# Kernel optimization log

Hardware: AMD Instinct MI355X
Metric: run time of the kernel (lower is better)

The kernel has to match this reference:

```python
import jax, jax.numpy as jnp
import numpy as np

B, N, DEG = 16, 2048, 16          # graphs, nodes per graph, avg out-degree
C_IN, HID, K = 64, 128, 32        # in_channels, hidden_channels, out_channels (clusters)
NT = B * N                        # total nodes
E = NT * DEG                      # total edges
GN_EPS = 1e-5


def setup_inputs() -> dict:
    key = jax.random.key(0)
    ks = jax.random.split(key, 6)
    x = jax.random.normal(ks[0], (NT, C_IN), jnp.float32)
    # within-graph random edges (sorted batch => node i belongs to graph i // N)
    src_l = jax.random.randint(ks[1], (E,), 0, N)
    dst_l = jax.random.randint(ks[2], (E,), 0, N)
    gid = jnp.repeat(jnp.arange(B, dtype=jnp.int32), N * DEG)
    edge_index = jnp.stack([gid * N + src_l, gid * N + dst_l]).astype(jnp.int32)
    batch = jnp.repeat(jnp.arange(B, dtype=jnp.int32), N)
    return dict(
        x=x, edge_index=edge_index, batch=batch,
        gn_weight=jnp.ones((C_IN,), jnp.float32),
        gn_bias=jnp.zeros((C_IN,), jnp.float32),
        gn_mean_scale=jnp.ones((C_IN,), jnp.float32),
        w1=jax.random.normal(ks[3], (C_IN, HID), jnp.float32) / np.float32(np.sqrt(C_IN)),
        b1=jnp.zeros((HID,), jnp.float32),
        w2=jax.random.normal(ks[4], (HID, K), jnp.float32) / np.float32(np.sqrt(HID)),
        b2=jnp.zeros((K,), jnp.float32),
    )


def reference(x, gn_weight, gn_bias, gn_mean_scale, w1, b1, w2, b2, edge_index, batch):
    # ---- GraphNorm (per-graph mean/var with learnable mean scale) ----
    ones_n = jnp.ones((NT,), x.dtype)
    cnt = jax.ops.segment_sum(ones_n, batch, num_segments=B)[:, None]        # [B,1]
    mean = jax.ops.segment_sum(x, batch, num_segments=B) / cnt              # [B,C]
    xm = x - gn_mean_scale * mean[batch]
    var = jax.ops.segment_sum(xm * xm, batch, num_segments=B) / cnt         # [B,C]
    h = gn_weight * xm / jnp.sqrt(var + GN_EPS)[batch] + gn_bias            # [NT,C_IN]

    # ---- GCNConv (add self-loops, symmetric D^-1/2 (A+I) D^-1/2) ----
    src, dst = edge_index[0], edge_index[1]
    loop = jnp.arange(NT, dtype=src.dtype)
    src_l = jnp.concatenate([src, loop])
    dst_l = jnp.concatenate([dst, loop])
    deg = jax.ops.segment_sum(jnp.ones_like(src_l, x.dtype), dst_l, num_segments=NT)
    dinv = jnp.where(deg > 0, jax.lax.rsqrt(deg), 0.0)
    norm = dinv[src_l] * dinv[dst_l]                                        # [E+NT]
    hw = h @ w1                                                             # [NT,HID]
    h = jax.ops.segment_sum(norm[:, None] * hw[src_l], dst_l, num_segments=NT) + b1
    h = jax.nn.selu(h)

    # ---- to_dense_batch / to_dense_adj (uniform graph sizes -> mask all True) ----
    xd = h.reshape(B, N, HID)                                               # [B,N,F]
    adj = jnp.zeros((B, N, N), x.dtype).at[batch[src], src % N, dst % N].add(1.0)

    # ---- DMoNPooling ----
    s = jax.nn.softmax(xd @ w2 + b2, axis=-1)                               # [B,N,K]
    out = jax.nn.selu(jnp.einsum('bnk,bnf->bkf', s, xd))                    # [B,K,F]
    sta = jnp.einsum('bnk,bnm->bkm', s, adj)                                # [B,K,N]
    out_adj = jnp.einsum('bkm,bml->bkl', sta, s)                            # [B,K,K]

    degrees = adj.sum(-1)                                                   # [B,N]
    m = degrees.sum(-1) / 2                                                 # [B]
    ca = jnp.einsum('bnk,bn->bk', s, degrees)                               # [B,K]
    normalizer = ca[:, :, None] * ca[:, None, :] / 2 / m[:, None, None]
    spectral_loss = (-jnp.einsum('bkk->b', out_adj - normalizer) / (2 * m)).mean()

    ss = jnp.einsum('bnk,bnl->bkl', s, s)                                   # [B,K,K]
    ss_fro = jnp.sqrt(jnp.sum(ss * ss, axis=(-2, -1), keepdims=True))
    eye = jnp.eye(K, dtype=x.dtype)
    diff = ss / ss_fro - eye / jnp.sqrt(jnp.float32(K))
    ortho_loss = jnp.sqrt(jnp.sum(diff * diff, axis=(-2, -1))).mean()

    cluster_size = s.sum(1)                                                 # [B,K]
    cluster_loss = (jnp.linalg.norm(cluster_size, axis=1) / N
                    * jnp.sqrt(jnp.float32(K)) - 1).mean()
    # (coarsened-adj renormalization in DMoNPooling is unused by Net's outputs)

    return jax.nn.log_softmax(out, axis=-1), spectral_loss + ortho_loss + cluster_loss, s
```

## Files before the change

kernel.cpp:

```cpp
#include <hip/hip_runtime.h>
#include <cmath>

static constexpr int B_  = 16;
static constexpr int N_  = 2048;
static constexpr int NT_ = 32768;
static constexpr int E_  = 524288;

static constexpr size_t OFF_HSC    = 0;
static constexpr size_t OFF_XD     = 2097152;
static constexpr size_t OFF_SWS    = 6291456;
static constexpr size_t OFF_PART   = 7340032;
static constexpr size_t OFF_GSP    = 9437184;
static constexpr size_t OFF_GSP2   = 9445376;
static constexpr size_t OFF_SSP    = 9453568;
static constexpr size_t OFF_CAP    = 9977856;
static constexpr size_t OFF_CSP    = 9994240;
static constexpr size_t OFF_SPECP  = 10010624;
static constexpr size_t OFF_DINV   = 10011136;
static constexpr size_t OFF_IHIN   = 10043904;
static constexpr size_t OFF_IHOUT  = 10306048;
static constexpr size_t OFF_ICURS  = 10568192;
static constexpr size_t OFF_IROWS  = 10830336;
static constexpr size_t OFF_ICNTO  = 10863108;
static constexpr size_t OFF_IESRC  = 10895876;

__device__ __forceinline__ float selu_f(float x) {
  return 1.0507009873554805f * (x > 0.f ? x : 1.6732632423543772f * expm1f(x));
}

__device__ __forceinline__ float block_sum_bcast(float v, float* sm) {
  int lane = threadIdx.x & 63, w = threadIdx.x >> 6;
#pragma unroll
  for (int off = 32; off; off >>= 1) v += __shfl_down(v, off);
  __syncthreads();
  if (lane == 0) sm[w] = v;
  __syncthreads();
  return sm[0] + sm[1] + sm[2] + sm[3];
}

__global__ __launch_bounds__(1024) void k_count(const int* ei, const float* x,
                                                int* histin, int* histout,
                                                float* gsp, float* gsp2) {
  __shared__ int hin[2048], hout[2048];
  __shared__ float l1[16][64], l2[16][64];
  int blk = blockIdx.x;
  int tid = threadIdx.x;
  if (blk < 128) {
    int g = blk >> 3, p = blk & 7;
    int nbase = g * 2048, ebase = g * 32768 + p * 4096;
    hin[tid] = 0; hin[tid + 1024] = 0;
    hout[tid] = 0; hout[tid + 1024] = 0;
    __syncthreads();
#pragma unroll
    for (int it = 0; it < 4; it++) {
      int e = ebase + it * 1024 + tid;
      int s = ei[e], d = ei[E_ + e];
      atomicAdd(&hout[s - nbase], 1);
      atomicAdd(&hin[d - nbase], 1);
    }
    __syncthreads();
    histin[blk * 2048 + tid] = hin[tid];
    histin[blk * 2048 + tid + 1024] = hin[tid + 1024];
    histout[blk * 2048 + tid] = hout[tid];
    histout[blk * 2048 + tid + 1024] = hout[tid + 1024];
  } else {
    int gi = blk - 128;
    int b = gi >> 3, chunk = gi & 7;
    int c = tid & 63, r = tid >> 6;
    float s = 0.f, s2 = 0.f;
    const float* xb = x + ((size_t)b * N_ + (size_t)chunk * 256) * 64;
    for (int n = r; n < 256; n += 16) {
      float v = xb[n * 64 + c];
      s += v; s2 += v * v;
    }
    l1[r][c] = s; l2[r][c] = s2;
    __syncthreads();
    if (r == 0) {
      float t1 = 0.f, t2 = 0.f;
#pragma unroll
      for (int i = 0; i < 16; i++) { t1 += l1[i][c]; t2 += l2[i][c]; }
      gsp[gi * 64 + c] = t1;
      gsp2[gi * 64 + c] = t2;
    }
  }
}

__global__ __launch_bounds__(1024) void k_scan(const int* histin, const int* histout,
                                               int* rows, int* cursp, int* cout_,
                                               float* dinv) {
  __shared__ int sb[1024];
  int g = blockIdx.x, tid = threadIdx.x;
  int nbase = g * 2048, ebase = g * 32768;
  int n0 = 2 * tid, n1 = 2 * tid + 1;
  int h0[8], h1[8];
  int a = 0, b = 0, o0 = 0, o1 = 0;
#pragma unroll
  for (int p = 0; p < 8; p++) {
    h0[p] = histin[(g * 8 + p) * 2048 + n0];
    h1[p] = histin[(g * 8 + p) * 2048 + n1];
    a += h0[p]; b += h1[p];
    o0 += histout[(g * 8 + p) * 2048 + n0];
    o1 += histout[(g * 8 + p) * 2048 + n1];
  }
  sb[tid] = a + b;
  __syncthreads();
  for (int off = 1; off < 1024; off <<= 1) {
    int add = (tid >= off) ? sb[tid - off] : 0;
    __syncthreads();
    sb[tid] += add;
    __syncthreads();
  }
  int pref = (tid > 0) ? sb[tid - 1] : 0;
  int r0 = ebase + pref, r1 = r0 + a;
  rows[nbase + n0] = r0;
  rows[nbase + n1] = r1;
  dinv[nbase + n0] = rsqrtf((float)(a + 1));
  dinv[nbase + n1] = rsqrtf((float)(b + 1));
  cout_[nbase + n0] = o0;
  cout_[nbase + n1] = o1;
  int run0 = r0, run1 = r1;
#pragma unroll
  for (int p = 0; p < 8; p++) {
    cursp[(g * 8 + p) * 2048 + n0] = run0; run0 += h0[p];
    cursp[(g * 8 + p) * 2048 + n1] = run1; run1 += h1[p];
  }
  if (g == 15 && tid == 1023) rows[NT_] = E_;
}

__global__ __launch_bounds__(256) void k_prepb(const float* x, const float* gsp,
                                               const float* gsp2, const float* gw,
                                               const float* gb, const float* gms,
                                               const float* dinv, float* hsc,
                                               const int* ei, const int* cursp,
                                               int* esrc) {
  __shared__ float shs[64], scs[64];
  __shared__ int cur[2048];
  int tid = threadIdx.x;
  int blk = blockIdx.x;
  if (blk < 2048) {
    int bgr = blk >> 7;
    if (tid < 64) {
      float s = 0.f, s2 = 0.f;
#pragma unroll
      for (int c8 = 0; c8 < 8; c8++) {
        s  += gsp[(bgr * 8 + c8) * 64 + tid];
        s2 += gsp2[(bgr * 8 + c8) * 64 + tid];
      }
      float mean = s * (1.f / 2048.f);
      float a = gms[tid];
      float var = s2 * (1.f / 2048.f) - (2.f * a - a * a) * mean * mean;
      shs[tid] = a * mean;
      scs[tid] = gw[tid] * rsqrtf(var + 1e-5f);
    }
    __syncthreads();
    int idx = blk * 256 + tid;
    int node = idx >> 4, g4 = (idx & 15) * 4;
    float di = dinv[node];
    float4 xv = *(const float4*)&x[(size_t)node * 64 + g4];
    float4 bb = *(const float4*)&gb[g4];
    float4 o;
    o.x = ((xv.x - shs[g4])     * scs[g4]     + bb.x) * di;
    o.y = ((xv.y - shs[g4 + 1]) * scs[g4 + 1] + bb.y) * di;
    o.z = ((xv.z - shs[g4 + 2]) * scs[g4 + 2] + bb.z) * di;
    o.w = ((xv.w - shs[g4 + 3]) * scs[g4 + 3] + bb.w) * di;
    *(float4*)&hsc[(size_t)node * 64 + g4] = o;
  } else {
    int bb = blk - 2048;
    int g = bb >> 3, p = bb & 7;
    int nbase = g * 2048;
    int ebase = g * 32768 + p * 4096;
    for (int i = tid; i < 2048; i += 256) cur[i] = cursp[bb * 2048 + i];
    __syncthreads();
#pragma unroll
    for (int it = 0; it < 16; it++) {
      int e = ebase + it * 256 + tid;
      int s = ei[e], d = ei[E_ + e];
      int pos = atomicAdd(&cur[d - nbase], 1);
      esrc[pos] = s;
    }
  }
}

__global__ __launch_bounds__(256) void k_mm1(const float* hsc, const float* dinv,
                                             const int* rows, const int* esrc,
                                             const float* w1, const float* b1,
                                             float* xd) {
  __shared__ float at[32 * 65];
  int tid = threadIdx.x;
  int n0 = blockIdx.x * 32;
  int wv = tid >> 6, c = tid & 63;
#pragma unroll 1
  for (int i = 0; i < 8; i++) {
    int nn = i * 4 + wv;
    int node = n0 + nn;
    int e0 = rows[node], e1 = rows[node + 1];
    float dd = dinv[node];
    float acc = hsc[(size_t)node * 64 + c];
    for (int e = e0; e < e1; e += 8) {
      int sidx[8]; float wt[8], hv[8];
#pragma unroll
      for (int j = 0; j < 8; j++) {
        int ee = e + j;
        sidx[j] = esrc[ee < e1 ? ee : e0];
        wt[j] = (ee < e1) ? 1.f : 0.f;
      }
#pragma unroll
      for (int j = 0; j < 8; j++) hv[j] = hsc[(size_t)sidx[j] * 64 + c];
#pragma unroll
      for (int j = 0; j < 8; j++) acc += wt[j] * hv[j];
    }
    at[nn * 65 + c] = dd * acc;
  }
  __syncthreads();
  int tx = tid & 31, ty = tid >> 5;
  int f0 = tx * 4, nn = ty * 4;
  float acc[4][4] = {};
  for (int k = 0; k < 64; k++) {
    float4 wvv = *(const float4*)&w1[k * 128 + f0];
#pragma unroll
    for (int i = 0; i < 4; i++) {
      float av = at[(nn + i) * 65 + k];
      acc[i][0] += av * wvv.x; acc[i][1] += av * wvv.y;
      acc[i][2] += av * wvv.z; acc[i][3] += av * wvv.w;
    }
  }
  float4 bv = *(const float4*)&b1[f0];
#pragma unroll
  for (int i = 0; i < 4; i++) {
    float4 o;
    o.x = selu_f(acc[i][0] + bv.x);
    o.y = selu_f(acc[i][1] + bv.y);
    o.z = selu_f(acc[i][2] + bv.z);
    o.w = selu_f(acc[i][3] + bv.w);
    *(float4*)&xd[(size_t)(n0 + nn + i) * 128 + f0] = o;
  }
}

__global__ __launch_bounds__(256) void k_mm2f(const float* xd, const float* w2,
                                              const float* b2, const int* cout_,
                                              float* s_ws, float* outs, float* ssp,
                                              float* cap, float* csp, float* part) {
  __shared__ float xt[64 * 129];
  __shared__ float st[64 * 33];
  __shared__ float r1[8][32], r2[8][32];
  int tid = threadIdx.x;
  int blk = blockIdx.x;
  int n0 = blk * 64;
  for (int i = tid; i < 2048; i += 256) {
    int n = i >> 5, j4 = (i & 31) * 4;
    float4 v = *(const float4*)&xd[(size_t)(n0 + n) * 128 + j4];
    xt[n * 129 + j4] = v.x; xt[n * 129 + j4 + 1] = v.y;
    xt[n * 129 + j4 + 2] = v.z; xt[n * 129 + j4 + 3] = v.w;
  }
  __syncthreads();
  int ty = tid >> 3;
  int k0 = (tid & 7) * 4;
  float acc2[2][4] = {};
  for (int j = 0; j < 128; j++) {
    float4 wv = *(const float4*)&w2[j * 32 + k0];
    float x0 = xt[(ty * 2) * 129 + j];
    float x1 = xt[(ty * 2 + 1) * 129 + j];
    acc2[0][0] += x0 * wv.x; acc2[0][1] += x0 * wv.y; acc2[0][2] += x0 * wv.z; acc2[0][3] += x0 * wv.w;
    acc2[1][0] += x1 * wv.x; acc2[1][1] += x1 * wv.y; acc2[1][2] += x1 * wv.z; acc2[1][3] += x1 * wv.w;
  }
  float4 bv2 = *(const float4*)&b2[k0];
#pragma unroll
  for (int i = 0; i < 2; i++) {
    int n = ty * 2 + i;
    st[n * 33 + k0]     = acc2[i][0] + bv2.x;
    st[n * 33 + k0 + 1] = acc2[i][1] + bv2.y;
    st[n * 33 + k0 + 2] = acc2[i][2] + bv2.z;
    st[n * 33 + k0 + 3] = acc2[i][3] + bv2.w;
  }
  __syncthreads();
  if (tid < 64) {
    float m = -3.4e38f;
    for (int kk = 0; kk < 32; kk++) m = fmaxf(m, st[tid * 33 + kk]);
    float ssum = 0.f;
    for (int kk = 0; kk < 32; kk++) {
      float e = expf(st[tid * 33 + kk] - m);
      st[tid * 33 + kk] = e; ssum += e;
    }
    float inv = 1.f / ssum;
    for (int kk = 0; kk < 32; kk++) st[tid * 33 + kk] *= inv;
  }
  __syncthreads();
  for (int i = tid; i < 512; i += 256) {
    int n = i >> 3, q = (i & 7) * 4;
    float4 o = {st[n * 33 + q], st[n * 33 + q + 1], st[n * 33 + q + 2], st[n * 33 + q + 3]};
    *(float4*)&s_ws[(size_t)(n0 + n) * 32 + q] = o;
    float* op = &outs[(size_t)(n0 + n) * 32 + q];
    op[0] = o.x; op[1] = o.y; op[2] = o.z; op[3] = o.w;
  }
  {
    int k = tid >> 3, l0 = (tid & 7) * 4;
    float a0 = 0, a1 = 0, a2 = 0, a3 = 0;
    for (int n = 0; n < 64; n++) {
      float sk = st[n * 33 + k];
      a0 += sk * st[n * 33 + l0];     a1 += sk * st[n * 33 + l0 + 1];
      a2 += sk * st[n * 33 + l0 + 2]; a3 += sk * st[n * 33 + l0 + 3];
    }
    float4 o = {a0, a1, a2, a3};
    *(float4*)&ssp[(size_t)blk * 1024 + k * 32 + l0] = o;
  }
  {
    int k2 = tid & 31, r = tid >> 5;
    float aca = 0.f, acs = 0.f;
    for (int i = 0; i < 8; i++) {
      int n = i * 8 + r;
      float dg = (float)cout_[n0 + n];
      float v = st[n * 33 + k2];
      acs += v; aca += v * dg;
    }
    r1[r][k2] = aca; r2[r][k2] = acs;
    __syncthreads();
    if (r == 0) {
      float sa = 0.f, sc = 0.f;
#pragma unroll
      for (int i = 0; i < 8; i++) { sa += r1[i][k2]; sc += r2[i][k2]; }
      cap[blk * 32 + k2] = sa;
      csp[blk * 32 + k2] = sc;
    }
  }
  {
    int tx = tid & 31, ty2 = tid >> 5;
    int f0 = tx * 4, kk0 = ty2 * 4;
    float acc[4][4] = {};
    for (int n = 0; n < 64; n++) {
      float s0 = st[n * 33 + kk0], s1 = st[n * 33 + kk0 + 1];
      float s2 = st[n * 33 + kk0 + 2], s3 = st[n * 33 + kk0 + 3];
      float4 xv = {xt[n * 129 + f0], xt[n * 129 + f0 + 1], xt[n * 129 + f0 + 2], xt[n * 129 + f0 + 3]};
      acc[0][0] += s0 * xv.x; acc[0][1] += s0 * xv.y; acc[0][2] += s0 * xv.z; acc[0][3] += s0 * xv.w;
      acc[1][0] += s1 * xv.x; acc[1][1] += s1 * xv.y; acc[1][2] += s1 * xv.z; acc[1][3] += s1 * xv.w;
      acc[2][0] += s2 * xv.x; acc[2][1] += s2 * xv.y; acc[2][2] += s2 * xv.z; acc[2][3] += s2 * xv.w;
      acc[3][0] += s3 * xv.x; acc[3][1] += s3 * xv.y; acc[3][2] += s3 * xv.z; acc[3][3] += s3 * xv.w;
    }
#pragma unroll
    for (int i = 0; i < 4; i++) {
      float4 o = {acc[i][0], acc[i][1], acc[i][2], acc[i][3]};
      *(float4*)&part[(size_t)(blk * 32 + kk0 + i) * 128 + f0] = o;
    }
  }
}

__global__ __launch_bounds__(256) void k_spec(const int* ei, const float* s_ws,
                                              float* specp, float* lossp) {
  __shared__ float sm4[4];
  int blk = blockIdx.x, tid = threadIdx.x;
  if (blk == 0 && tid == 0) lossp[0] = 0.f;
  int ebase = blk * 1024;
  float acc = 0.f;
#pragma unroll
  for (int j = 0; j < 4; j++) {
    int e = ebase + j * 256 + tid;
    int s = ei[e], d = ei[E_ + e];
    const float4* ap = (const float4*)&s_ws[(size_t)s * 32];
    const float4* cp = (const float4*)&s_ws[(size_t)d * 32];
#pragma unroll
    for (int q = 0; q < 8; q++) {
      float4 u = ap[q], v = cp[q];
      acc += u.x * v.x + u.y * v.y + u.z * v.z + u.w * v.w;
    }
  }
  int lane = tid & 63, w = tid >> 6;
#pragma unroll
  for (int off = 32; off; off >>= 1) acc += __shfl_down(acc, off);
  if (lane == 0) sm4[w] = acc;
  __syncthreads();
  if (tid == 0) specp[blk] = sm4[0] + sm4[1] + sm4[2] + sm4[3];
}

__global__ __launch_bounds__(256) void k_fin2(const float* part, const float* ssp,
                                              const float* csp, const float* cap,
                                              const float* specp, float* out0,
                                              float* loss) {
  __shared__ float sred[4];
  int blk = blockIdx.x;
  int tid = threadIdx.x;
  if (blk < 256) {
    int half = tid >> 7;
    int f = tid & 127;
    int row = blk * 2 + half;
    int b = row >> 5, k = row & 31;
    float v = 0.f;
#pragma unroll
    for (int c = 0; c < 32; c++) v += part[(size_t)((b * 32 + c) * 32 + k) * 128 + f];
    v = selu_f(v);
    int lane = tid & 63, w = tid >> 6;
    float m = v;
#pragma unroll
    for (int off = 32; off; off >>= 1) m = fmaxf(m, __shfl_down(m, off));
    if (lane == 0) sred[w] = m;
    __syncthreads();
    m = fmaxf(sred[half * 2], sred[half * 2 + 1]);
    float e = expf(v - m);
    float t = e;
    __syncthreads();
#pragma unroll
    for (int off = 32; off; off >>= 1) t += __shfl_down(t, off);
    if (lane == 0) sred[w] = t;
    __syncthreads();
    float tot = sred[half * 2] + sred[half * 2 + 1];
    out0[(size_t)row * 128 + f] = v - m - logf(tot);
  } else {
    int b = blk - 256;
    float v0 = 0, v1 = 0, v2 = 0, v3 = 0;
    for (int c = 0; c < 32; c++) {
      float4 u = *(const float4*)&ssp[(size_t)(b * 32 + c) * 1024 + tid * 4];
      v0 += u.x; v1 += u.y; v2 += u.z; v3 += u.w;
    }
    float ssq = v0 * v0 + v1 * v1 + v2 * v2 + v3 * v3;
    ssq = block_sum_bcast(ssq, sred);
    float inv = 1.f / sqrtf(ssq);
    float dsq = 0.f;
    {
      int i0 = tid * 4;
      float vv[4] = {v0, v1, v2, v3};
#pragma unroll
      for (int jj = 0; jj < 4; jj++) {
        int i = i0 + jj;
        float d = vv[jj] * inv;
        if ((i >> 5) == (i & 31)) d -= 0.17677669529663687f;
        dsq += d * d;
      }
    }
    dsq = block_sum_bcast(dsq, sred);
    float csq = 0.f, casq = 0.f;
    if (tid < 32) {
      float c1 = 0.f, c2 = 0.f;
      for (int c = 0; c < 32; c++) {
        c1 += csp[(size_t)(b * 32 + c) * 32 + tid];
        c2 += cap[(size_t)(b * 32 + c) * 32 + tid];
      }
      csq = c1 * c1; casq = c2 * c2;
    }
    csq = block_sum_bcast(csq, sred);
    casq = block_sum_bcast(casq, sred);
    float spec_sum = (tid < 32) ? specp[b * 32 + tid] : 0.f;
    spec_sum = block_sum_bcast(spec_sum, sred);
    if (tid == 0) {
      float ortho = sqrtf(dsq);
      float cl = sqrtf(csq) * (1.f / 2048.f) * 5.656854249492381f - 1.f;
      float m = 16384.f;
      float spec = -(spec_sum - casq / (2.f * m)) / (2.f * m);
      atomicAdd(loss, (spec + ortho + cl) * (1.f / 16.f));
    }
  }
}

extern "C" void kernel_launch(void* const* d_in, const int* in_sizes, int n_in,
                              void* d_out, int out_size, void* d_ws, size_t ws_size,
                              hipStream_t stream) {
  (void)in_sizes; (void)n_in; (void)out_size; (void)ws_size;
  const float* x   = (const float*)d_in[0];
  const int*   ei  = (const int*)d_in[1];
  const float* gw  = (const float*)d_in[3];
  const float* gb  = (const float*)d_in[4];
  const float* gms = (const float*)d_in[5];
  const float* w1  = (const float*)d_in[6];
  const float* b1  = (const float*)d_in[7];
  const float* w2  = (const float*)d_in[8];
  const float* b2  = (const float*)d_in[9];
  float* out = (float*)d_out;
  float* ws  = (float*)d_ws;

  float* hsc    = ws + OFF_HSC;
  float* xd     = ws + OFF_XD;
  float* s_ws   = ws + OFF_SWS;
  float* part   = ws + OFF_PART;
  float* gsp    = ws + OFF_GSP;
  float* gsp2   = ws + OFF_GSP2;
  float* ssp    = ws + OFF_SSP;
  float* cap    = ws + OFF_CAP;
  float* csp    = ws + OFF_CSP;
  float* specp  = ws + OFF_SPECP;
  float* dinv   = ws + OFF_DINV;
  int*   histin = (int*)(ws + OFF_IHIN);
  int*   histout= (int*)(ws + OFF_IHOUT);
  int*   cursp  = (int*)(ws + OFF_ICURS);
  int*   rows   = (int*)(ws + OFF_IROWS);
  int*   cout_  = (int*)(ws + OFF_ICNTO);
  int*   esrc   = (int*)(ws + OFF_IESRC);

  float* out0  = out;
  float* lossp = out + 65536;
  float* outs  = out + 65537;

  hipLaunchKernelGGL(k_count, dim3(256), dim3(1024), 0, stream, ei, x, histin, histout, gsp, gsp2);
  hipLaunchKernelGGL(k_scan, dim3(16), dim3(1024), 0, stream,
                     histin, histout, rows, cursp, cout_, dinv);
  hipLaunchKernelGGL(k_prepb, dim3(2176), dim3(256), 0, stream,
                     x, gsp, gsp2, gw, gb, gms, dinv, hsc, ei, cursp, esrc);
  hipLaunchKernelGGL(k_mm1, dim3(1024), dim3(256), 0, stream, hsc, dinv, rows, esrc, w1, b1, xd);
  hipLaunchKernelGGL(k_mm2f, dim3(512), dim3(256), 0, stream,
                     xd, w2, b2, cout_, s_ws, outs, ssp, cap, csp, part);
  hipLaunchKernelGGL(k_spec, dim3(512), dim3(256), 0, stream, ei, s_ws, specp, lossp);
  hipLaunchKernelGGL(k_fin2, dim3(272), dim3(256), 0, stream,
                     part, ssp, csp, cap, specp, out0, lossp);
}
```

Before: 201.9 us.

## Use CSR gather for spectral term, warp-shuffle scan and parallel softmax

The spectral trace term now walks the destination-sorted CSR (rows/esrc) with one 32-lane group per node. Each lane gathers one cluster column of the source rows, replacing the per-edge reads of two full 128-byte s rows from the raw edge list. The s matrix is read straight from the output buffer, which drops the extra s_ws copy. The block scan in k_scan now uses wavefront shuffles instead of a barrier-heavy Hillis-Steele loop, and the row softmax in k_mm2f is split across 4 threads per row with shuffle reductions. The spec partials double to 1024 blocks and fin2 is adjusted to match; the CSR walk adds per-node imbalance and padded inner loops.

```diff
diff --git a/kernel.cpp b/kernel.cpp
--- a/kernel.cpp
+++ b/kernel.cpp
@@ -15,7 +15,6 @@
 static constexpr size_t OFF_SSP    = 9453568;
 static constexpr size_t OFF_CAP    = 9977856;
 static constexpr size_t OFF_CSP    = 9994240;
-static constexpr size_t OFF_SPECP  = 10010624;
 static constexpr size_t OFF_DINV   = 10011136;
 static constexpr size_t OFF_IHIN   = 10043904;
 static constexpr size_t OFF_IHOUT  = 10306048;
@@ -88,7 +87,7 @@
 __global__ __launch_bounds__(1024) void k_scan(const int* histin, const int* histout,
                                                int* rows, int* cursp, int* cout_,
                                                float* dinv) {
-  __shared__ int sb[1024];
+  __shared__ int wsum[16], woff[16];
   int g = blockIdx.x, tid = threadIdx.x;
   int nbase = g * 2048, ebase = g * 32768;
   int n0 = 2 * tid, n1 = 2 * tid + 1;
@@ -102,15 +101,27 @@
     o0 += histout[(g * 8 + p) * 2048 + n0];
     o1 += histout[(g * 8 + p) * 2048 + n1];
   }
-  sb[tid] = a + b;
-  __syncthreads();
-  for (int off = 1; off < 1024; off <<= 1) {
-    int add = (tid >= off) ? sb[tid - off] : 0;
-    __syncthreads();
-    sb[tid] += add;
-    __syncthreads();
-  }
-  int pref = (tid > 0) ? sb[tid - 1] : 0;
+  int tot = a + b;
+  int lane = tid & 63, w = tid >> 6;
+  int incl = tot;
+#pragma unroll
+  for (int off = 1; off < 64; off <<= 1) {
+    int t = __shfl_up(incl, off);
+    if (lane >= off) incl += t;
+  }
+  if (lane == 63) wsum[w] = incl;
+  __syncthreads();
+  if (tid < 16) {
+    int v = wsum[tid], iv = v;
+#pragma unroll
+    for (int off = 1; off < 16; off <<= 1) {
+      int t = __shfl_up(iv, off, 16);
+      if (tid >= off) iv += t;
+    }
+    woff[tid] = iv - v;
+  }
+  __syncthreads();
+  int pref = incl - tot + woff[w];
   int r0 = ebase + pref, r1 = r0 + a;
   rows[nbase + n0] = r0;
   rows[nbase + n1] = r1;
@@ -238,7 +249,7 @@
 
 __global__ __launch_bounds__(256) void k_mm2f(const float* xd, const float* w2,
                                               const float* b2, const int* cout_,
-                                              float* s_ws, float* outs, float* ssp,
+                                              float* outs, float* ssp,
                                               float* cap, float* csp, float* part) {
   __shared__ float xt[64 * 129];
   __shared__ float st[64 * 33];
@@ -273,24 +284,30 @@
     st[n * 33 + k0 + 3] = acc2[i][3] + bv2.w;
   }
   __syncthreads();
-  if (tid < 64) {
+  {
+    int n = tid >> 2, q = (tid & 3) * 8;
     float m = -3.4e38f;
-    for (int kk = 0; kk < 32; kk++) m = fmaxf(m, st[tid * 33 + kk]);
-    float ssum = 0.f;
-    for (int kk = 0; kk < 32; kk++) {
-      float e = expf(st[tid * 33 + kk] - m);
-      st[tid * 33 + kk] = e; ssum += e;
-    }
+#pragma unroll
+    for (int j = 0; j < 8; j++) m = fmaxf(m, st[n * 33 + q + j]);
+#pragma unroll
+    for (int off = 1; off < 4; off <<= 1) m = fmaxf(m, __shfl_xor(m, off, 4));
+    float ev[8]; float ssum = 0.f;
+#pragma unroll
+    for (int j = 0; j < 8; j++) { ev[j] = expf(st[n * 33 + q + j] - m); ssum += ev[j]; }
+#pragma unroll
+    for (int off = 1; off < 4; off <<= 1) ssum += __shfl_xor(ssum, off, 4);
     float inv = 1.f / ssum;
-    for (int kk = 0; kk < 32; kk++) st[tid * 33 + kk] *= inv;
+#pragma unroll
+    for (int j = 0; j < 8; j++) st[n * 33 + q + j] = ev[j] * inv;
   }
   __syncthreads();
   for (int i = tid; i < 512; i += 256) {
     int n = i >> 3, q = (i & 7) * 4;
-    float4 o = {st[n * 33 + q], st[n * 33 + q + 1], st[n * 33 + q + 2], st[n * 33 + q + 3]};
-    *(float4*)&s_ws[(size_t)(n0 + n) * 32 + q] = o;
     float* op = &outs[(size_t)(n0 + n) * 32 + q];
-    op[0] = o.x; op[1] = o.y; op[2] = o.z; op[3] = o.w;
+    op[0] = st[n * 33 + q];
+    op[1] = st[n * 33 + q + 1];
+    op[2] = st[n * 33 + q + 2];
+    op[3] = st[n * 33 + q + 3];
   }
   {
     int k = tid >> 3, l0 = (tid & 7) * 4;
@@ -343,31 +360,44 @@
   }
 }
 
-__global__ __launch_bounds__(256) void k_spec(const int* ei, const float* s_ws,
-                                              float* specp, float* lossp) {
-  __shared__ float sm4[4];
+__global__ __launch_bounds__(256) void k_spec(const int* rows, const int* esrc,
+                                              const float* s, float* specp,
+                                              float* lossp) {
+  __shared__ float sm8[8];
   int blk = blockIdx.x, tid = threadIdx.x;
   if (blk == 0 && tid == 0) lossp[0] = 0.f;
-  int ebase = blk * 1024;
+  int grp = tid >> 5, k = tid & 31;
+  int n0 = blk * 32 + grp * 4;
   float acc = 0.f;
-#pragma unroll
-  for (int j = 0; j < 4; j++) {
-    int e = ebase + j * 256 + tid;
-    int s = ei[e], d = ei[E_ + e];
-    const float4* ap = (const float4*)&s_ws[(size_t)s * 32];
-    const float4* cp = (const float4*)&s_ws[(size_t)d * 32];
-#pragma unroll
-    for (int q = 0; q < 8; q++) {
-      float4 u = ap[q], v = cp[q];
-      acc += u.x * v.x + u.y * v.y + u.z * v.z + u.w * v.w;
-    }
-  }
-  int lane = tid & 63, w = tid >> 6;
-#pragma unroll
-  for (int off = 32; off; off >>= 1) acc += __shfl_down(acc, off);
-  if (lane == 0) sm4[w] = acc;
-  __syncthreads();
-  if (tid == 0) specp[blk] = sm4[0] + sm4[1] + sm4[2] + sm4[3];
+#pragma unroll 1
+  for (int i = 0; i < 4; i++) {
+    int node = n0 + i;
+    int e0 = rows[node], e1 = rows[node + 1];
+    float sd = s[(size_t)node * 32 + k];
+    float agg = 0.f;
+    for (int e = e0; e < e1; e += 4) {
+      int si[4]; float wt[4], sv[4];
+#pragma unroll
+      for (int j = 0; j < 4; j++) {
+        int ee = e + j;
+        si[j] = esrc[ee < e1 ? ee : e0];
+        wt[j] = (ee < e1) ? 1.f : 0.f;
+      }
+#pragma unroll
+      for (int j = 0; j < 4; j++) sv[j] = s[(size_t)si[j] * 32 + k];
+#pragma unroll
+      for (int j = 0; j < 4; j++) agg += wt[j] * sv[j];
+    }
+    acc += sd * agg;
+  }
+#pragma unroll
+  for (int off = 16; off; off >>= 1) acc += __shfl_down(acc, off, 32);
+  if (k == 0) sm8[grp] = acc;
+  __syncthreads();
+  if (tid == 0) {
+    specp[blk] = sm8[0] + sm8[1] + sm8[2] + sm8[3]
+               + sm8[4] + sm8[5] + sm8[6] + sm8[7];
+  }
 }
 
 __global__ __launch_bounds__(256) void k_fin2(const float* part, const float* ssp,
@@ -436,7 +466,7 @@
     }
     csq = block_sum_bcast(csq, sred);
     casq = block_sum_bcast(casq, sred);
-    float spec_sum = (tid < 32) ? specp[b * 32 + tid] : 0.f;
+    float spec_sum = (tid < 64) ? specp[b * 64 + tid] : 0.f;
     spec_sum = block_sum_bcast(spec_sum, sred);
     if (tid == 0) {
       float ortho = sqrtf(dsq);
@@ -466,14 +496,13 @@
 
   float* hsc    = ws + OFF_HSC;
   float* xd     = ws + OFF_XD;
-  float* s_ws   = ws + OFF_SWS;
   float* part   = ws + OFF_PART;
   float* gsp    = ws + OFF_GSP;
   float* gsp2   = ws + OFF_GSP2;
   float* ssp    = ws + OFF_SSP;
   float* cap    = ws + OFF_CAP;
   float* csp    = ws + OFF_CSP;
-  float* specp  = ws + OFF_SPECP;
+  float* specp  = ws + OFF_SWS;
   float* dinv   = ws + OFF_DINV;
   int*   histin = (int*)(ws + OFF_IHIN);
   int*   histout= (int*)(ws + OFF_IHOUT);
@@ -493,8 +522,8 @@
                      x, gsp, gsp2, gw, gb, gms, dinv, hsc, ei, cursp, esrc);
   hipLaunchKernelGGL(k_mm1, dim3(1024), dim3(256), 0, stream, hsc, dinv, rows, esrc, w1, b1, xd);
   hipLaunchKernelGGL(k_mm2f, dim3(512), dim3(256), 0, stream,
-                     xd, w2, b2, cout_, s_ws, outs, ssp, cap, csp, part);
-  hipLaunchKernelGGL(k_spec, dim3(512), dim3(256), 0, stream, ei, s_ws, specp, lossp);
+                     xd, w2, b2, cout_, outs, ssp, cap, csp, part);
+  hipLaunchKernelGGL(k_spec, dim3(1024), dim3(256), 0, stream, rows, esrc, outs, specp, lossp);
   hipLaunchKernelGGL(k_fin2, dim3(272), dim3(256), 0, stream,
                      part, ssp, csp, cap, specp, out0, lossp);
 }
```

Result: no change. 199.7 us (-1.1%).
